# Kernel optimization log

Hardware: AMD Instinct MI355X
Metric: run time of the kernel (lower is better)

Reference implementation:

```python
import jax, jax.numpy as jnp
import numpy as np

L, N, E, D = 4, 50000, 250000, 128
EPS = 1e-5

def _ln(h, g, b):
    mu = jnp.mean(h, axis=-1, keepdims=True)
    var = jnp.mean(jnp.square(h - mu), axis=-1, keepdims=True)
    return (h - mu) * jax.lax.rsqrt(var + EPS) * g + b

def setup_inputs() -> dict:
    key = jax.random.key(0)
    ks = jax.random.split(key, 8)
    s1 = 1.0 / np.sqrt(3 * D)
    s2 = 1.0 / np.sqrt(D)
    s3 = 1.0 / np.sqrt(2 * D)
    return {
        "x": jax.random.normal(ks[0], (N, D), jnp.float32),
        "edge_index": jax.random.randint(ks[1], (2, E), 0, N, jnp.int32),
        "edge_attr": jax.random.normal(ks[2], (E, D), jnp.float32),
        "eW1": jax.random.normal(ks[3], (L, 3 * D, D), jnp.float32) * s1,
        "eb1": jnp.zeros((L, D), jnp.float32),
        "eW2": jax.random.normal(ks[4], (L, D, D), jnp.float32) * s2,
        "eb2": jnp.zeros((L, D), jnp.float32),
        "eG": jnp.ones((L, D), jnp.float32),
        "eB": jnp.zeros((L, D), jnp.float32),
        "nW1": jax.random.normal(ks[5], (L, 2 * D, D), jnp.float32) * s3,
        "nb1": jnp.zeros((L, D), jnp.float32),
        "nW2": jax.random.normal(ks[6], (L, D, D), jnp.float32) * s2,
        "nb2": jnp.zeros((L, D), jnp.float32),
        "nG": jnp.ones((L, D), jnp.float32),
        "nB": jnp.zeros((L, D), jnp.float32),
    }

def reference(x, edge_index, edge_attr, eW1, eb1, eW2, eb2, eG, eB,
              nW1, nb1, nW2, nb2, nG, nB):
    src = edge_index[0]  # scatter target (custom aggregate uses edge_index[0])
    dst = edge_index[1]  # x_i under PyG source_to_target flow
    n_nodes = x.shape[0]

    def step(carry, p):
        xc, ea = carry
        ew1, eb1_, ew2, eb2_, eg, ebt, nw1, nb1_, nw2, nb2_, ng, nbt = p
        # message: cat(x_i, x_j, edge_attr) -> MLP -> residual
        m = jnp.concatenate([xc[dst], xc[src], ea], axis=1)  # [E, 3D]
        h = jax.nn.relu(m @ ew1 + eb1_) @ ew2 + eb2_
        ea_new = ea + _ln(h, eg, ebt)
        # aggregate: scatter-sum edges into nodes by edge_index[0]
        agg = jax.ops.segment_sum(ea_new, src, num_segments=n_nodes)  # [N, D]
        # update: cat(x, agg) -> MLP -> residual
        u = jnp.concatenate([xc, agg], axis=1)  # [N, 2D]
        h2 = jax.nn.relu(u @ nw1 + nb1_) @ nw2 + nb2_
        x_new = xc + _ln(h2, ng, nbt)
        return (x_new, ea_new), None

    (x_out, ea_out), _ = jax.lax.scan(
        step, (x, edge_attr),
        (eW1, eb1, eW2, eb2, eG, eB, nW1, nb1, nW2, nb2, nG, nB))
    return x_out, ea_out
```

## Files before the change

kernel.cpp:

```cpp
#include <hip/hip_runtime.h>
#include <hip/hip_bf16.h>

#define N_NODES 50000
#define N_EDGES 250000
#define DIM 128
#define LAYERS 4
#define LN_EPS 1e-5f

typedef __hip_bfloat16 bf16;
typedef float f32x4 __attribute__((ext_vector_type(4)));
typedef __bf16 bfx8 __attribute__((ext_vector_type(8)));
typedef unsigned short u16x8 __attribute__((ext_vector_type(8)));

#define F_X   0
#define F_EA  1
#define F_EW1 2
#define F_EW2 3
#define F_EG  4
#define F_NW1 5
#define F_NW2 6
#define F_NG  7

__device__ __forceinline__ float b2f(bf16 v) { return __bfloat162float(v); }
__device__ __forceinline__ bf16  f2b(float v) { return __float2bfloat16(v); }
__device__ __forceinline__ unsigned short f2us(float v) {
    return __builtin_bit_cast(unsigned short, __float2bfloat16(v));
}

__device__ __forceinline__ float ldv(const void* p, size_t i, int f) {
    if (f) return ((const float*)p)[i];
    else   return b2f(((const bf16*)p)[i]);
}
__device__ __forceinline__ void stv(void* p, size_t i, float v, int f) {
    if (f) ((float*)p)[i] = v;
    else   ((bf16*)p)[i] = f2b(v);
}

__device__ __forceinline__ bfx8 cvt8(f32x4 lo, f32x4 hi) {
    u16x8 u;
    #pragma unroll
    for (int i = 0; i < 4; i++) { u[i] = f2us(lo[i]); u[i + 4] = f2us(hi[i]); }
    return __builtin_bit_cast(bfx8, u);
}

__device__ __forceinline__ void mfma8(const bf16* pBk, bfx8 a, f32x4* acc) {
    #pragma unroll
    for (int f = 0; f < 8; f++) {
        bfx8 b = *reinterpret_cast<const bfx8*>(pBk + f * 128);
        acc[f] = __builtin_amdgcn_mfma_f32_16x16x32_bf16(a, b, acc[f], 0, 0, 0);
    }
}

__global__ void k_detect(const void* x, const void* ea,
                         const void* eW1, const void* eW2,
                         const void* nW1, const void* nW2,
                         const void* eG, const void* nG,
                         int* flags)
{
    __shared__ int bad[6];
    const void* ptrs[6] = { x, ea, eW1, eW2, nW1, nW2 };
    const int t = threadIdx.x;
    if (t < 6) bad[t] = 0;
    __syncthreads();
    for (int b = 0; b < 6; b++) {
        const bf16* p = (const bf16*)ptrs[b];
        int isbad = 0;
        for (int i = t; i < 4096; i += 256) {
            float v = b2f(p[i]);
            if (!(fabsf(v) < 1e4f)) isbad = 1;
        }
        if (isbad) atomicOr(&bad[b], 1);
    }
    __syncthreads();
    if (t == 0) {
        flags[F_X]   = bad[0];
        flags[F_EA]  = bad[1];
        flags[F_EW1] = bad[2];
        flags[F_EW2] = bad[3];
        flags[F_NW1] = bad[4];
        flags[F_NW2] = bad[5];
        const bf16* g1 = (const bf16*)eG;
        const bf16* g2 = (const bf16*)nG;
        flags[F_EG] = (b2f(g1[0]) == 1.0f && b2f(g1[1]) == 1.0f) ? 0 : 1;
        flags[F_NG] = (b2f(g2[0]) == 1.0f && b2f(g2[1]) == 1.0f) ? 0 : 1;
    }
}

__global__ void k_init_x(const void* __restrict__ x_in, float* __restrict__ xf,
                         bf16* __restrict__ xb, const int* __restrict__ flags) {
    const int f = flags[F_X];
    size_t i = (size_t)blockIdx.x * 256 + threadIdx.x;
    if (i < (size_t)N_NODES * DIM) {
        float v = ldv(x_in, i, f);
        xf[i] = v;
        xb[i] = f2b(v);
    }
}

__global__ void k_init_ea(const void* __restrict__ ea_in, void* __restrict__ d_out,
                          const int* __restrict__ flags) {
    const int fe = flags[F_EA];
    const int fo = flags[F_X];
    void* ea = fo ? (void*)((float*)d_out + (size_t)N_NODES * DIM)
                  : (void*)((bf16*)d_out + (size_t)N_NODES * DIM);
    size_t i = (size_t)blockIdx.x * 256 + threadIdx.x;
    if (i < (size_t)N_EDGES * DIM) stv(ea, i, ldv(ea_in, i, fe), fo);
}

__global__ void k_wprep(const void* __restrict__ W, bf16* __restrict__ Wb,
                        int K, const int* __restrict__ flags, int fidx)
{
    const int f = flags[fidx];
    size_t i = (size_t)blockIdx.x * 256 + threadIdx.x;
    const int per = K * DIM;
    if (i >= (size_t)LAYERS * per) return;
    int l   = (int)(i / per);
    int rem = (int)(i % per);
    int j   = rem & 7;
    int c   = (rem >> 3) & 127;
    int kq  = rem >> 10;
    int k   = kq * 8 + j;
    Wb[i] = f2b(ldv(W, (size_t)l * per + (size_t)k * DIM + c, f));
}

__global__ __launch_bounds__(256)
void k_edge(const bf16* __restrict__ xb,
            void* __restrict__ d_out,
            const int* __restrict__ srcI, const int* __restrict__ dstI,
            const bf16* __restrict__ W1b, const bf16* __restrict__ W2b,
            const void* __restrict__ b1, const void* __restrict__ b2,
            const void* __restrict__ G,  const void* __restrict__ B,
            float* __restrict__ agg,
            const int* __restrict__ flags, int layer)
{
    __shared__ alignas(16) bf16 h_s[4][16 * DIM];

    const int fo = flags[F_X];
    const int fg = flags[F_EG];

    void* ea = fo ? (void*)((float*)d_out + (size_t)N_NODES * DIM)
                  : (void*)((bf16*)d_out + (size_t)N_NODES * DIM);

    const bf16* W1l = W1b + (size_t)layer * 3 * DIM * DIM;
    const bf16* W2l = W2b + (size_t)layer * DIM * DIM;
    const bf16* b1l = (const bf16*)b1 + (size_t)layer * DIM;
    const bf16* b2l = (const bf16*)b2 + (size_t)layer * DIM;
    const bf16* Bl  = (const bf16*)B  + (size_t)layer * DIM;
    const void* Gl  = fg ? (const void*)((const float*)G + (size_t)layer * DIM)
                         : (const void*)((const bf16*)G  + (size_t)layer * DIM);

    const int tid  = threadIdx.x;
    const int wv   = tid >> 6;
    const int lane = tid & 63;
    const int cl   = lane & 15;
    const int kp   = lane >> 4;

    const int e0w = blockIdx.x * 64 + wv * 16;

    const int eA = (e0w + cl < N_EDGES) ? (e0w + cl) : (N_EDGES - 1);
    const bf16* pAd = xb + (size_t)dstI[eA] * DIM + kp * 8;
    const bf16* pAs = xb + (size_t)srcI[eA] * DIM + kp * 8;
    const bf16* pB  = W1l + kp * 1024 + cl * 8;

    f32x4 acc[8];
    #pragma unroll
    for (int f = 0; f < 8; f++) acc[f] = (f32x4){0.f, 0.f, 0.f, 0.f};

    #pragma unroll
    for (int kk = 0; kk < 4; kk++)
        mfma8(pB + (size_t)kk * 4096,
              *reinterpret_cast<const bfx8*>(pAd + kk * 32), acc);
    #pragma unroll
    for (int kk = 0; kk < 4; kk++)
        mfma8(pB + (size_t)(kk + 4) * 4096,
              *reinterpret_cast<const bfx8*>(pAs + kk * 32), acc);
    if (fo) {
        const float* pAe = (const float*)ea + (size_t)eA * DIM + kp * 8;
        #pragma unroll
        for (int kk = 0; kk < 4; kk++) {
            f32x4 lo = *reinterpret_cast<const f32x4*>(pAe + kk * 32);
            f32x4 hi = *reinterpret_cast<const f32x4*>(pAe + kk * 32 + 4);
            mfma8(pB + (size_t)(kk + 8) * 4096, cvt8(lo, hi), acc);
        }
    } else {
        const bf16* pAe = (const bf16*)ea + (size_t)eA * DIM + kp * 8;
        #pragma unroll
        for (int kk = 0; kk < 4; kk++)
            mfma8(pB + (size_t)(kk + 8) * 4096,
                  *reinterpret_cast<const bfx8*>(pAe + kk * 32), acc);
    }

    char* hb = (char*)h_s + wv * (16 * DIM * 2);
    #pragma unroll
    for (int f = 0; f < 8; f++) {
        const int col = f * 16 + cl;
        const float bias1 = b2f(b1l[col]);
        #pragma unroll
        for (int j = 0; j < 4; j++) {
            const int r = kp * 4 + j;
            float hv = fmaxf(acc[f][j] + bias1, 0.f);
            *(bf16*)(hb + r * 256 + ((col * 2) ^ ((r & 7) << 4))) = f2b(hv);
        }
    }
    __syncthreads();

    const bf16* pB2 = W2l + kp * 1024 + cl * 8;
    f32x4 acc2[8];
    #pragma unroll
    for (int f = 0; f < 8; f++) acc2[f] = (f32x4){0.f, 0.f, 0.f, 0.f};
    #pragma unroll
    for (int kk = 0; kk < 4; kk++) {
        bfx8 a = *reinterpret_cast<const bfx8*>(
            hb + cl * 256 + ((kk * 64 + kp * 16) ^ ((cl & 7) << 4)));
        mfma8(pB2 + (size_t)kk * 4096, a, acc2);
    }

    float g_[8], be_[8];
    #pragma unroll
    for (int f = 0; f < 8; f++) {
        const int col = f * 16 + cl;
        const float bias2 = b2f(b2l[col]);
        #pragma unroll
        for (int j = 0; j < 4; j++) acc2[f][j] += bias2;
        g_[f]  = ldv(Gl, col, fg);
        be_[f] = b2f(Bl[col]);
    }
    float mu[4], rs[4];
    #pragma unroll
    for (int j = 0; j < 4; j++) {
        float s = 0.f, q = 0.f;
        #pragma unroll
        for (int f = 0; f < 8; f++) { float v = acc2[f][j]; s += v; q += v * v; }
        #pragma unroll
        for (int m = 1; m <= 8; m <<= 1) { s += __shfl_xor(s, m); q += __shfl_xor(q, m); }
        mu[j] = s * (1.f / DIM);
        float var = q * (1.f / DIM) - mu[j] * mu[j];
        rs[j] = rsqrtf(var + LN_EPS);
    }

    int eR[4], sR[4], vR[4];
    #pragma unroll
    for (int j = 0; j < 4; j++) {
        int e = e0w + kp * 4 + j;
        vR[j] = (e < N_EDGES);
        eR[j] = vR[j] ? e : (N_EDGES - 1);
        sR[j] = srcI[eR[j]];
    }
    #pragma unroll
    for (int f = 0; f < 8; f++) {
        const int col = f * 16 + cl;
        #pragma unroll
        for (int j = 0; j < 4; j++) {
            if (!vR[j]) continue;
            const float val = (acc2[f][j] - mu[j]) * rs[j] * g_[f] + be_[f];
            const size_t off = (size_t)eR[j] * DIM + col;
            const float ean = ldv(ea, off, fo) + val;
            stv(ea, off, ean, fo);
            atomicAdd(&agg[(size_t)sR[j] * DIM + col], ean);
        }
    }
}

__global__ __launch_bounds__(256)
void k_node(float* __restrict__ xf, bf16* __restrict__ xb,
            float* __restrict__ agg,
            void* __restrict__ d_out,
            const bf16* __restrict__ W1b, const bf16* __restrict__ W2b,
            const void* __restrict__ b1, const void* __restrict__ b2,
            const void* __restrict__ G,  const void* __restrict__ B,
            const int* __restrict__ flags, int layer)
{
    __shared__ alignas(16) bf16 h_s[4][16 * DIM];

    const int fo = flags[F_X];
    const int fg = flags[F_NG];

    const bf16* W1l = W1b + (size_t)layer * 2 * DIM * DIM;
    const bf16* W2l = W2b + (size_t)layer * DIM * DIM;
    const bf16* b1l = (const bf16*)b1 + (size_t)layer * DIM;
    const bf16* b2l = (const bf16*)b2 + (size_t)layer * DIM;
    const bf16* Bl  = (const bf16*)B  + (size_t)layer * DIM;
    const void* Gl  = fg ? (const void*)((const float*)G + (size_t)layer * DIM)
                         : (const void*)((const bf16*)G  + (size_t)layer * DIM);

    const int tid  = threadIdx.x;
    const int wv   = tid >> 6;
    const int lane = tid & 63;
    const int cl   = lane & 15;
    const int kp   = lane >> 4;

    const int n0w = blockIdx.x * 64 + wv * 16;
    const int nA  = (n0w + cl < N_NODES) ? (n0w + cl) : (N_NODES - 1);

    const bf16*  pAx = xb  + (size_t)nA * DIM + kp * 8;
    const float* pAg = agg + (size_t)nA * DIM + kp * 8;
    const bf16*  pB  = W1l + kp * 1024 + cl * 8;

    f32x4 acc[8];
    #pragma unroll
    for (int f = 0; f < 8; f++) acc[f] = (f32x4){0.f, 0.f, 0.f, 0.f};

    #pragma unroll
    for (int kk = 0; kk < 4; kk++)
        mfma8(pB + (size_t)kk * 4096,
              *reinterpret_cast<const bfx8*>(pAx + kk * 32), acc);
    #pragma unroll
    for (int kk = 0; kk < 4; kk++) {
        f32x4 lo = *reinterpret_cast<const f32x4*>(pAg + kk * 32);
        f32x4 hi = *reinterpret_cast<const f32x4*>(pAg + kk * 32 + 4);
        mfma8(pB + (size_t)(kk + 4) * 4096, cvt8(lo, hi), acc);
    }

    char* hb = (char*)h_s + wv * (16 * DIM * 2);
    #pragma unroll
    for (int f = 0; f < 8; f++) {
        const int col = f * 16 + cl;
        const float bias1 = b2f(b1l[col]);
        #pragma unroll
        for (int j = 0; j < 4; j++) {
            const int r = kp * 4 + j;
            float hv = fmaxf(acc[f][j] + bias1, 0.f);
            *(bf16*)(hb + r * 256 + ((col * 2) ^ ((r & 7) << 4))) = f2b(hv);
        }
    }
    __syncthreads();

    const bf16* pB2 = W2l + kp * 1024 + cl * 8;
    f32x4 acc2[8];
    #pragma unroll
    for (int f = 0; f < 8; f++) acc2[f] = (f32x4){0.f, 0.f, 0.f, 0.f};
    #pragma unroll
    for (int kk = 0; kk < 4; kk++) {
        bfx8 a = *reinterpret_cast<const bfx8*>(
            hb + cl * 256 + ((kk * 64 + kp * 16) ^ ((cl & 7) << 4)));
        mfma8(pB2 + (size_t)kk * 4096, a, acc2);
    }

    float g_[8], be_[8];
    #pragma unroll
    for (int f = 0; f < 8; f++) {
        const int col = f * 16 + cl;
        const float bias2 = b2f(b2l[col]);
        #pragma unroll
        for (int j = 0; j < 4; j++) acc2[f][j] += bias2;
        g_[f]  = ldv(Gl, col, fg);
        be_[f] = b2f(Bl[col]);
    }
    float mu[4], rs[4];
    #pragma unroll
    for (int j = 0; j < 4; j++) {
        float s = 0.f, q = 0.f;
        #pragma unroll
        for (int f = 0; f < 8; f++) { float v = acc2[f][j]; s += v; q += v * v; }
        #pragma unroll
        for (int m = 1; m <= 8; m <<= 1) { s += __shfl_xor(s, m); q += __shfl_xor(q, m); }
        mu[j] = s * (1.f / DIM);
        float var = q * (1.f / DIM) - mu[j] * mu[j];
        rs[j] = rsqrtf(var + LN_EPS);
    }

    int nR[4], vR[4];
    #pragma unroll
    for (int j = 0; j < 4; j++) {
        int n = n0w + kp * 4 + j;
        vR[j] = (n < N_NODES);
        nR[j] = vR[j] ? n : (N_NODES - 1);
    }
    #pragma unroll
    for (int f = 0; f < 8; f++) {
        const int col = f * 16 + cl;
        #pragma unroll
        for (int j = 0; j < 4; j++) {
            if (!vR[j]) continue;
            const float val = (acc2[f][j] - mu[j]) * rs[j] * g_[f] + be_[f];
            const size_t off = (size_t)nR[j] * DIM + col;
            const float xn = xf[off] + val;
            xf[off] = xn;
            xb[off] = f2b(xn);
            stv(d_out, off, xn, fo);
            agg[off] = 0.f;
        }
    }
}

extern "C" void kernel_launch(void* const* d_in, const int* in_sizes, int n_in,
                              void* d_out, int out_size, void* d_ws, size_t ws_size,
                              hipStream_t stream)
{
    (void)in_sizes; (void)n_in; (void)out_size; (void)ws_size;
    const void* x_in  = d_in[0];
    const int*  ei    = (const int*)d_in[1];
    const void* ea_in = d_in[2];
    const void* eW1 = d_in[3];  const void* eb1 = d_in[4];
    const void* eW2 = d_in[5];  const void* eb2 = d_in[6];
    const void* eG  = d_in[7];  const void* eB  = d_in[8];
    const void* nW1 = d_in[9];  const void* nb1 = d_in[10];
    const void* nW2 = d_in[11]; const void* nb2 = d_in[12];
    const void* nG  = d_in[13]; const void* nB  = d_in[14];

    char* ws = (char*)d_ws;
    int*   flags = (int*)ws;
    float* agg = (float*)(ws + 256);
    float* xf  = (float*)(ws + 256 + (size_t)N_NODES * DIM * 4);
    bf16*  xb  = (bf16*) (ws + 256 + (size_t)N_NODES * DIM * 8);
    bf16*  eW1b = (bf16*)(ws + 256 + (size_t)N_NODES * DIM * 10);
    bf16*  eW2b = eW1b + (size_t)LAYERS * 3 * DIM * DIM;
    bf16*  nW1b = eW2b + (size_t)LAYERS * DIM * DIM;
    bf16*  nW2b = nW1b + (size_t)LAYERS * 2 * DIM * DIM;

    const int* srcI = ei;
    const int* dstI = ei + N_EDGES;

    k_detect<<<1, 256, 0, stream>>>(x_in, ea_in, eW1, eW2, nW1, nW2, eG, nG, flags);
    k_init_x<<<(N_NODES * DIM + 255) / 256, 256, 0, stream>>>(x_in, xf, xb, flags);
    k_init_ea<<<(int)(((size_t)N_EDGES * DIM + 255) / 256), 256, 0, stream>>>(ea_in, d_out, flags);
    k_wprep<<<(LAYERS * 3 * DIM * DIM + 255) / 256, 256, 0, stream>>>(eW1, eW1b, 3 * DIM, flags, F_EW1);
    k_wprep<<<(LAYERS * DIM * DIM + 255) / 256, 256, 0, stream>>>(eW2, eW2b, DIM, flags, F_EW2);
    k_wprep<<<(LAYERS * 2 * DIM * DIM + 255) / 256, 256, 0, stream>>>(nW1, nW1b, 2 * DIM, flags, F_NW1);
    k_wprep<<<(LAYERS * DIM * DIM + 255) / 256, 256, 0, stream>>>(nW2, nW2b, DIM, flags, F_NW2);
    hipMemsetAsync(agg, 0, (size_t)N_NODES * DIM * sizeof(float), stream);

    for (int l = 0; l < LAYERS; l++) {
        k_edge<<<(N_EDGES + 63) / 64, 256, 0, stream>>>(
            xb, d_out, srcI, dstI, eW1b, eW2b, eb1, eb2, eG, eB, agg, flags, l);
        k_node<<<(N_NODES + 63) / 64, 256, 0, stream>>>(
            xf, xb, agg, d_out, nW1b, nW2b, nb1, nb2, nG, nB, flags, l);
    }
}
```

Before: 1.483 ms.

## Replace atomic scatter aggregation with CSR gather in node kernel and vectorize stores

```diff
diff --git a/kernel.cpp b/kernel.cpp
--- a/kernel.cpp
+++ b/kernel.cpp
@@ -11,6 +11,8 @@
 typedef float f32x4 __attribute__((ext_vector_type(4)));
 typedef __bf16 bfx8 __attribute__((ext_vector_type(8)));
 typedef unsigned short u16x8 __attribute__((ext_vector_type(8)));
+typedef unsigned short u16x4 __attribute__((ext_vector_type(4)));
+typedef unsigned int   u32x4 __attribute__((ext_vector_type(4)));
 
 #define F_X   0
 #define F_EA  1
@@ -25,6 +27,9 @@
 __device__ __forceinline__ bf16  f2b(float v) { return __float2bfloat16(v); }
 __device__ __forceinline__ unsigned short f2us(float v) {
     return __builtin_bit_cast(unsigned short, __float2bfloat16(v));
+}
+__device__ __forceinline__ float us2f(unsigned short u) {
+    return __builtin_bit_cast(float, (unsigned)u << 16);
 }
 
 __device__ __forceinline__ float ldv(const void* p, size_t i, int f) {
@@ -89,22 +94,57 @@
 __global__ void k_init_x(const void* __restrict__ x_in, float* __restrict__ xf,
                          bf16* __restrict__ xb, const int* __restrict__ flags) {
     const int f = flags[F_X];
-    size_t i = (size_t)blockIdx.x * 256 + threadIdx.x;
-    if (i < (size_t)N_NODES * DIM) {
-        float v = ldv(x_in, i, f);
-        xf[i] = v;
-        xb[i] = f2b(v);
-    }
+    size_t i = ((size_t)blockIdx.x * 256 + threadIdx.x) * 4;
+    if (i >= (size_t)N_NODES * DIM) return;
+    f32x4 v;
+    if (f) {
+        v = *(const f32x4*)((const float*)x_in + i);
+    } else {
+        u16x4 u = *(const u16x4*)((const unsigned short*)x_in + i);
+        #pragma unroll
+        for (int q = 0; q < 4; q++) v[q] = us2f(u[q]);
+    }
+    *(f32x4*)(xf + i) = v;
+    u16x4 ub;
+    #pragma unroll
+    for (int q = 0; q < 4; q++) ub[q] = f2us(v[q]);
+    *(u16x4*)((unsigned short*)xb + i) = ub;
 }
 
 __global__ void k_init_ea(const void* __restrict__ ea_in, void* __restrict__ d_out,
                           const int* __restrict__ flags) {
     const int fe = flags[F_EA];
     const int fo = flags[F_X];
-    void* ea = fo ? (void*)((float*)d_out + (size_t)N_NODES * DIM)
-                  : (void*)((bf16*)d_out + (size_t)N_NODES * DIM);
-    size_t i = (size_t)blockIdx.x * 256 + threadIdx.x;
-    if (i < (size_t)N_EDGES * DIM) stv(ea, i, ldv(ea_in, i, fe), fo);
+    size_t i = ((size_t)blockIdx.x * 256 + threadIdx.x) * 4;
+    if (i >= (size_t)N_EDGES * DIM) return;
+    if (fe == fo) {
+        if (fo) {
+            float* d = (float*)d_out + (size_t)N_NODES * DIM;
+            *(u32x4*)(d + i) = *(const u32x4*)((const float*)ea_in + i);
+        } else {
+            bf16* d = (bf16*)d_out + (size_t)N_NODES * DIM;
+            *(u16x4*)((unsigned short*)d + i) =
+                *(const u16x4*)((const unsigned short*)ea_in + i);
+        }
+    } else {
+        f32x4 v;
+        if (fe) v = *(const f32x4*)((const float*)ea_in + i);
+        else {
+            u16x4 u = *(const u16x4*)((const unsigned short*)ea_in + i);
+            #pragma unroll
+            for (int q = 0; q < 4; q++) v[q] = us2f(u[q]);
+        }
+        if (fo) {
+            float* d = (float*)d_out + (size_t)N_NODES * DIM;
+            *(f32x4*)(d + i) = v;
+        } else {
+            bf16* d = (bf16*)d_out + (size_t)N_NODES * DIM;
+            u16x4 ub;
+            #pragma unroll
+            for (int q = 0; q < 4; q++) ub[q] = f2us(v[q]);
+            *(u16x4*)((unsigned short*)d + i) = ub;
+        }
+    }
 }
 
 __global__ void k_wprep(const void* __restrict__ W, bf16* __restrict__ Wb,
@@ -123,6 +163,41 @@
     Wb[i] = f2b(ldv(W, (size_t)l * per + (size_t)k * DIM + c, f));
 }
 
+__global__ void k_deg(const int* __restrict__ srcI, int* __restrict__ deg) {
+    int e = blockIdx.x * 256 + threadIdx.x;
+    if (e < N_EDGES) atomicAdd(&deg[srcI[e]], 1);
+}
+
+#define SCH ((N_NODES + 255) / 256)
+__global__ void k_scan(const int* __restrict__ deg, int* __restrict__ off,
+                       int* __restrict__ cur) {
+    __shared__ int part[256];
+    const int t = threadIdx.x;
+    const int lo = t * SCH;
+    const int hi = (lo + SCH < N_NODES) ? (lo + SCH) : N_NODES;
+    int s = 0;
+    for (int i = lo; i < hi; i++) s += deg[i];
+    part[t] = s;
+    __syncthreads();
+    if (t == 0) {
+        int run = 0;
+        for (int i = 0; i < 256; i++) { int v = part[i]; part[i] = run; run += v; }
+    }
+    __syncthreads();
+    int run = part[t];
+    for (int i = lo; i < hi; i++) { off[i] = run; cur[i] = run; run += deg[i]; }
+    if (hi == N_NODES) off[N_NODES] = run;
+}
+
+__global__ void k_fill(const int* __restrict__ srcI, int* __restrict__ cur,
+                       int* __restrict__ lst) {
+    int e = blockIdx.x * 256 + threadIdx.x;
+    if (e < N_EDGES) {
+        int p = atomicAdd(&cur[srcI[e]], 1);
+        lst[p] = e;
+    }
+}
+
 __global__ __launch_bounds__(256)
 void k_edge(const bf16* __restrict__ xb,
             void* __restrict__ d_out,
@@ -130,10 +205,9 @@
             const bf16* __restrict__ W1b, const bf16* __restrict__ W2b,
             const void* __restrict__ b1, const void* __restrict__ b2,
             const void* __restrict__ G,  const void* __restrict__ B,
-            float* __restrict__ agg,
             const int* __restrict__ flags, int layer)
 {
-    __shared__ alignas(16) bf16 h_s[4][16 * DIM];
+    __shared__ alignas(16) float smem[4][16 * 132];
 
     const int fo = flags[F_X];
     const int fg = flags[F_EG];
@@ -156,8 +230,7 @@
     const int kp   = lane >> 4;
 
     const int e0w = blockIdx.x * 64 + wv * 16;
-
-    const int eA = (e0w + cl < N_EDGES) ? (e0w + cl) : (N_EDGES - 1);
+    const int eA  = (e0w + cl < N_EDGES) ? (e0w + cl) : (N_EDGES - 1);
     const bf16* pAd = xb + (size_t)dstI[eA] * DIM + kp * 8;
     const bf16* pAs = xb + (size_t)srcI[eA] * DIM + kp * 8;
     const bf16* pB  = W1l + kp * 1024 + cl * 8;
@@ -190,7 +263,7 @@
                   *reinterpret_cast<const bfx8*>(pAe + kk * 32), acc);
     }
 
-    char* hb = (char*)h_s + wv * (16 * DIM * 2);
+    char* hb = (char*)&smem[wv][0];
     #pragma unroll
     for (int f = 0; f < 8; f++) {
         const int col = f * 16 + cl;
@@ -202,7 +275,6 @@
             *(bf16*)(hb + r * 256 + ((col * 2) ^ ((r & 7) << 4))) = f2b(hv);
         }
     }
-    __syncthreads();
 
     const bf16* pB2 = W2l + kp * 1024 + cl * 8;
     f32x4 acc2[8];
@@ -238,39 +310,49 @@
         rs[j] = rsqrtf(var + LN_EPS);
     }
 
-    int eR[4], sR[4], vR[4];
-    #pragma unroll
-    for (int j = 0; j < 4; j++) {
-        int e = e0w + kp * 4 + j;
-        vR[j] = (e < N_EDGES);
-        eR[j] = vR[j] ? e : (N_EDGES - 1);
-        sR[j] = srcI[eR[j]];
-    }
-    #pragma unroll
-    for (int f = 0; f < 8; f++) {
-        const int col = f * 16 + cl;
+    float* vs = &smem[wv][0];
+    #pragma unroll
+    for (int f = 0; f < 8; f++) {
         #pragma unroll
         for (int j = 0; j < 4; j++) {
-            if (!vR[j]) continue;
             const float val = (acc2[f][j] - mu[j]) * rs[j] * g_[f] + be_[f];
-            const size_t off = (size_t)eR[j] * DIM + col;
-            const float ean = ldv(ea, off, fo) + val;
-            stv(ea, off, ean, fo);
-            atomicAdd(&agg[(size_t)sR[j] * DIM + col], ean);
+            vs[(kp * 4 + j) * 132 + f * 16 + cl] = val;
+        }
+    }
+    const int lr = lane >> 5;
+    const int lc = (lane & 31) * 4;
+    #pragma unroll
+    for (int i = 0; i < 8; i++) {
+        const int r2 = 2 * i + lr;
+        const int e  = e0w + r2;
+        if (e >= N_EDGES) continue;
+        f32x4 v = *(const f32x4*)&vs[r2 * 132 + lc];
+        const size_t off = (size_t)e * DIM + lc;
+        if (fo) {
+            float* pe = (float*)ea + off;
+            f32x4 o = *(const f32x4*)pe;
+            *(f32x4*)pe = o + v;
+        } else {
+            bf16* pe = (bf16*)ea + off;
+            u16x4 uo = *(const u16x4*)(unsigned short*)pe;
+            u16x4 un;
+            #pragma unroll
+            for (int q = 0; q < 4; q++) un[q] = f2us(us2f(uo[q]) + v[q]);
+            *(u16x4*)(unsigned short*)pe = un;
         }
     }
 }
 
 __global__ __launch_bounds__(256)
 void k_node(float* __restrict__ xf, bf16* __restrict__ xb,
-            float* __restrict__ agg,
             void* __restrict__ d_out,
+            const int* __restrict__ off_, const int* __restrict__ lst,
             const bf16* __restrict__ W1b, const bf16* __restrict__ W2b,
             const void* __restrict__ b1, const void* __restrict__ b2,
             const void* __restrict__ G,  const void* __restrict__ B,
             const int* __restrict__ flags, int layer)
 {
-    __shared__ alignas(16) bf16 h_s[4][16 * DIM];
+    __shared__ alignas(16) float smem[4][16 * 132];
 
     const int fo = flags[F_X];
     const int fg = flags[F_NG];
@@ -292,9 +374,45 @@
     const int n0w = blockIdx.x * 64 + wv * 16;
     const int nA  = (n0w + cl < N_NODES) ? (n0w + cl) : (N_NODES - 1);
 
-    const bf16*  pAx = xb  + (size_t)nA * DIM + kp * 8;
-    const float* pAg = agg + (size_t)nA * DIM + kp * 8;
-    const bf16*  pB  = W1l + kp * 1024 + cl * 8;
+    f32x4 agl[4], agh[4];
+    #pragma unroll
+    for (int kk = 0; kk < 4; kk++) {
+        agl[kk] = (f32x4){0.f, 0.f, 0.f, 0.f};
+        agh[kk] = (f32x4){0.f, 0.f, 0.f, 0.f};
+    }
+    {
+        const int beg = off_[nA], end = off_[nA + 1];
+        if (fo) {
+            const float* base = (const float*)d_out + (size_t)N_NODES * DIM;
+            for (int idx = beg; idx < end; ++idx) {
+                const int e = lst[idx];
+                const float* p = base + (size_t)e * DIM + kp * 8;
+                #pragma unroll
+                for (int kk = 0; kk < 4; kk++) {
+                    agl[kk] += *(const f32x4*)(p + kk * 32);
+                    agh[kk] += *(const f32x4*)(p + kk * 32 + 4);
+                }
+            }
+        } else {
+            const bf16* base = (const bf16*)d_out + (size_t)N_NODES * DIM;
+            for (int idx = beg; idx < end; ++idx) {
+                const int e = lst[idx];
+                const bf16* p = base + (size_t)e * DIM + kp * 8;
+                #pragma unroll
+                for (int kk = 0; kk < 4; kk++) {
+                    u16x8 u = *(const u16x8*)(const unsigned short*)(p + kk * 32);
+                    #pragma unroll
+                    for (int q = 0; q < 4; q++) {
+                        agl[kk][q] += us2f(u[q]);
+                        agh[kk][q] += us2f(u[q + 4]);
+                    }
+                }
+            }
+        }
+    }
+
+    const bf16* pAx = xb + (size_t)nA * DIM + kp * 8;
+    const bf16* pB  = W1l + kp * 1024 + cl * 8;
 
     f32x4 acc[8];
     #pragma unroll
@@ -305,13 +423,10 @@
         mfma8(pB + (size_t)kk * 4096,
               *reinterpret_cast<const bfx8*>(pAx + kk * 32), acc);
     #pragma unroll
-    for (int kk = 0; kk < 4; kk++) {
-        f32x4 lo = *reinterpret_cast<const f32x4*>(pAg + kk * 32);
-        f32x4 hi = *reinterpret_cast<const f32x4*>(pAg + kk * 32 + 4);
-        mfma8(pB + (size_t)(kk + 4) * 4096, cvt8(lo, hi), acc);
-    }
-
-    char* hb = (char*)h_s + wv * (16 * DIM * 2);
+    for (int kk = 0; kk < 4; kk++)
+        mfma8(pB + (size_t)(kk + 4) * 4096, cvt8(agl[kk], agh[kk]), acc);
+
+    char* hb = (char*)&smem[wv][0];
     #pragma unroll
     for (int f = 0; f < 8; f++) {
         const int col = f * 16 + cl;
@@ -323,7 +438,6 @@
             *(bf16*)(hb + r * 256 + ((col * 2) ^ ((r & 7) << 4))) = f2b(hv);
         }
     }
-    __syncthreads();
 
     const bf16* pB2 = W2l + kp * 1024 + cl * 8;
     f32x4 acc2[8];
@@ -359,26 +473,35 @@
         rs[j] = rsqrtf(var + LN_EPS);
     }
 
-    int nR[4], vR[4];
-    #pragma unroll
-    for (int j = 0; j < 4; j++) {
-        int n = n0w + kp * 4 + j;
-        vR[j] = (n < N_NODES);
-        nR[j] = vR[j] ? n : (N_NODES - 1);
-    }
-    #pragma unroll
-    for (int f = 0; f < 8; f++) {
-        const int col = f * 16 + cl;
+    float* vs = &smem[wv][0];
+    #pragma unroll
+    for (int f = 0; f < 8; f++) {
         #pragma unroll
         for (int j = 0; j < 4; j++) {
-            if (!vR[j]) continue;
             const float val = (acc2[f][j] - mu[j]) * rs[j] * g_[f] + be_[f];
-            const size_t off = (size_t)nR[j] * DIM + col;
-            const float xn = xf[off] + val;
-            xf[off] = xn;
-            xb[off] = f2b(xn);
-            stv(d_out, off, xn, fo);
-            agg[off] = 0.f;
+            vs[(kp * 4 + j) * 132 + f * 16 + cl] = val;
+        }
+    }
+    const bool wout = (layer == LAYERS - 1);
+    const int lr = lane >> 5;
+    const int lc = (lane & 31) * 4;
+    #pragma unroll
+    for (int i = 0; i < 8; i++) {
+        const int r2 = 2 * i + lr;
+        const int n2 = n0w + r2;
+        if (n2 >= N_NODES) continue;
+        f32x4 v = *(const f32x4*)&vs[r2 * 132 + lc];
+        const size_t off = (size_t)n2 * DIM + lc;
+        f32x4 xo = *(const f32x4*)&xf[off];
+        f32x4 xn = xo + v;
+        *(f32x4*)&xf[off] = xn;
+        u16x4 ub;
+        #pragma unroll
+        for (int q = 0; q < 4; q++) ub[q] = f2us(xn[q]);
+        *(u16x4*)((unsigned short*)xb + off) = ub;
+        if (wout) {
+            if (fo) *(f32x4*)((float*)d_out + off) = xn;
+            else    *(u16x4*)((unsigned short*)(bf16*)d_out + off) = ub;
         }
     }
 }
@@ -399,31 +522,39 @@
     const void* nG  = d_in[13]; const void* nB  = d_in[14];
 
     char* ws = (char*)d_ws;
-    int*   flags = (int*)ws;
-    float* agg = (float*)(ws + 256);
-    float* xf  = (float*)(ws + 256 + (size_t)N_NODES * DIM * 4);
-    bf16*  xb  = (bf16*) (ws + 256 + (size_t)N_NODES * DIM * 8);
-    bf16*  eW1b = (bf16*)(ws + 256 + (size_t)N_NODES * DIM * 10);
-    bf16*  eW2b = eW1b + (size_t)LAYERS * 3 * DIM * DIM;
-    bf16*  nW1b = eW2b + (size_t)LAYERS * DIM * DIM;
-    bf16*  nW2b = nW1b + (size_t)LAYERS * 2 * DIM * DIM;
+    int* flags = (int*)ws;
+    char* p = ws + 256;
+    float* xf  = (float*)p;  p += (size_t)N_NODES * DIM * 4;
+    bf16*  xb  = (bf16*)p;   p += (size_t)N_NODES * DIM * 2;
+    bf16*  eW1b = (bf16*)p;  p += (size_t)LAYERS * 3 * DIM * DIM * 2;
+    bf16*  eW2b = (bf16*)p;  p += (size_t)LAYERS * DIM * DIM * 2;
+    bf16*  nW1b = (bf16*)p;  p += (size_t)LAYERS * 2 * DIM * DIM * 2;
+    bf16*  nW2b = (bf16*)p;  p += (size_t)LAYERS * DIM * DIM * 2;
+    int* deg     = (int*)p;  p += 200000;
+    int* csr_off = (int*)p;  p += 200016;
+    int* cur     = (int*)p;  p += 200000;
+    int* lst     = (int*)p;  p += 1000000;
 
     const int* srcI = ei;
     const int* dstI = ei + N_EDGES;
 
     k_detect<<<1, 256, 0, stream>>>(x_in, ea_in, eW1, eW2, nW1, nW2, eG, nG, flags);
-    k_init_x<<<(N_NODES * DIM + 255) / 256, 256, 0, stream>>>(x_in, xf, xb, flags);
-    k_init_ea<<<(int)(((size_t)N_EDGES * DIM + 255) / 256), 256, 0, stream>>>(ea_in, d_out, flags);
+    k_init_x<<<(N_NODES * DIM / 4 + 255) / 256, 256, 0, stream>>>(x_in, xf, xb, flags);
+    k_init_ea<<<(int)(((size_t)N_EDGES * DIM / 4 + 255) / 256), 256, 0, stream>>>(ea_in, d_out, flags);
     k_wprep<<<(LAYERS * 3 * DIM * DIM + 255) / 256, 256, 0, stream>>>(eW1, eW1b, 3 * DIM, flags, F_EW1);
     k_wprep<<<(LAYERS * DIM * DIM + 255) / 256, 256, 0, stream>>>(eW2, eW2b, DIM, flags, F_EW2);
     k_wprep<<<(LAYERS * 2 * DIM * DIM + 255) / 256, 256, 0, stream>>>(nW1, nW1b, 2 * DIM, flags, F_NW1);
     k_wprep<<<(LAYERS * DIM * DIM + 255) / 256, 256, 0, stream>>>(nW2, nW2b, DIM, flags, F_NW2);
-    hipMemsetAsync(agg, 0, (size_t)N_NODES * DIM * sizeof(float), stream);
+
+    hipMemsetAsync(deg, 0, N_NODES * sizeof(int), stream);
+    k_deg<<<(N_EDGES + 255) / 256, 256, 0, stream>>>(srcI, deg);
+    k_scan<<<1, 256, 0, stream>>>(deg, csr_off, cur);
+    k_fill<<<(N_EDGES + 255) / 256, 256, 0, stream>>>(srcI, cur, lst);
 
     for (int l = 0; l < LAYERS; l++) {
         k_edge<<<(N_EDGES + 63) / 64, 256, 0, stream>>>(
-            xb, d_out, srcI, dstI, eW1b, eW2b, eb1, eb2, eG, eB, agg, flags, l);
+            xb, d_out, srcI, dstI, eW1b, eW2b, eb1, eb2, eG, eB, flags, l);
         k_node<<<(N_NODES + 63) / 64, 256, 0, stream>>>(
-            xf, xb, agg, d_out, nW1b, nW2b, nb1, nb2, nG, nB, flags, l);
-    }
-}
+            xf, xb, d_out, csr_off, lst, nW1b, nW2b, nb1, nb2, nG, nB, flags, l);
+    }
+}
```

Result: faster. 1.392 ms (-6.1%).
